# Performance work log

Measured on AMD Instinct MI355X. Metric: run time of the kernel, lower is better.

The kernel has to match this reference:

```python
import jax, jax.numpy as jnp
import numpy as np

N, E, F_IN, H, D = 50000, 800000, 256, 4, 128


def _gat_layer(x, W, al, ar, bias, src, dst):
    # x: [N, Fin]; W: [Fin, H*D]; al/ar: [H, D]; bias: [H*D]
    feat = (x @ W).reshape(N, H, D)                      # [N,H,D]
    el = jnp.einsum('nhd,hd->nh', feat, al)              # [N,H]
    er = jnp.einsum('nhd,hd->nh', feat, ar)              # [N,H]
    e = jax.nn.leaky_relu(el[src] + er[dst], negative_slope=0.2)  # [E,H]
    # edge softmax over incoming edges of each dst node (numerically stable)
    emax = jax.ops.segment_max(e, dst, num_segments=N)   # [N,H]
    ee = jnp.exp(e - emax[dst])                          # [E,H]
    denom = jax.ops.segment_sum(ee, dst, num_segments=N) # [N,H]
    a = ee / denom[dst]                                  # [E,H]
    # weighted scatter-aggregate of source features
    out = jax.ops.segment_sum(feat[src] * a[:, :, None], dst, num_segments=N)  # [N,H,D]
    return out + bias.reshape(H, D)


def setup_inputs() -> dict:
    key = jax.random.key(0)
    ks = jax.random.split(key, 16)
    f32 = jnp.float32
    nfeats = jax.random.normal(ks[0], (N, F_IN), dtype=f32)
    src = jax.random.randint(ks[1], (E,), 0, N, dtype=jnp.int32)
    dst = jax.random.randint(ks[2], (E,), 0, N, dtype=jnp.int32)
    def lin(k, fin):
        return jax.random.normal(k, (fin, H * D), dtype=f32) / np.sqrt(fin).astype(np.float32)
    def attn(k):
        return jax.random.normal(k, (H, D), dtype=f32) / np.sqrt(D).astype(np.float32)
    return {
        'nfeats': nfeats,
        'W1': lin(ks[3], F_IN), 'al1': attn(ks[4]), 'ar1': attn(ks[5]), 'b1': jnp.zeros((H * D,), f32),
        'W2': lin(ks[6], D),    'al2': attn(ks[7]), 'ar2': attn(ks[8]), 'b2': jnp.zeros((H * D,), f32),
        'W3': lin(ks[9], D),    'al3': attn(ks[10]), 'ar3': attn(ks[11]), 'b3': jnp.zeros((H * D,), f32),
        'Wc': jax.random.normal(ks[12], (D, 1), dtype=f32) / np.sqrt(D).astype(np.float32),
        'bc': jnp.zeros((1,), f32),
        'src': src, 'dst': dst,
    }


def reference(nfeats, W1, al1, ar1, b1, W2, al2, ar2, b2, W3, al3, ar3, b3, Wc, bc, src, dst):
    h = jnp.mean(jax.nn.relu(_gat_layer(nfeats, W1, al1, ar1, b1, src, dst)), axis=1)  # [N,D]
    h = jnp.mean(jax.nn.relu(_gat_layer(h, W2, al2, ar2, b2, src, dst)), axis=1)
    h = jnp.mean(jax.nn.relu(_gat_layer(h, W3, al3, ar3, b3, src, dst)), axis=1)
    hg = jnp.mean(h, axis=0, keepdims=True)  # readout: mean over nodes -> [1,D]
    return jax.nn.sigmoid(hg @ Wc + bc)      # [1,1]
```

## Files before the change

kernel.cpp:

```cpp
#include <hip/hip_runtime.h>
#include <hip/hip_bf16.h>

#define N_NODES 50000
#define E_EDGES 800000
#define HD 512
#define H_HEADS 4
#define D_DIM 128
#define N_PAD 53248

typedef __attribute__((ext_vector_type(8))) short bf16x8;
typedef __attribute__((ext_vector_type(4))) float f32x4;
typedef __attribute__((ext_vector_type(2))) float f32x2;

__device__ __forceinline__ unsigned short f2b(float f) {
  unsigned u = __float_as_uint(f);
  u += 0x7FFFu + ((u >> 16) & 1u);
  return (unsigned short)(u >> 16);
}
__device__ __forceinline__ float b2f(unsigned short s) {
  return __uint_as_float(((unsigned)s) << 16);
}
__device__ __forceinline__ float lrelu(float v) { return v > 0.f ? v : 0.2f * v; }
__device__ __forceinline__ float sel4(float a, float b, float c, float d, int h) {
  return h == 0 ? a : (h == 1 ? b : (h == 2 ? c : d));
}
__device__ __forceinline__ float sel4v(float4 v, int h) {
  return sel4(v.x, v.y, v.z, v.w, h);
}

#define GLOAD_LDS16(g, l)                                             \
  __builtin_amdgcn_global_load_lds(                                   \
      (const __attribute__((address_space(1))) void*)(g),             \
      (__attribute__((address_space(3))) void*)(l), 16, 0, 0)

__global__ void cast_f2b(const float* __restrict__ in, unsigned short* __restrict__ out, int n4) {
  int i = blockIdx.x * blockDim.x + threadIdx.x;
  if (i >= n4) return;
  float4 v = *(const float4*)(in + (size_t)i * 4);
  ushort4 o;
  o.x = f2b(v.x); o.y = f2b(v.y); o.z = f2b(v.z); o.w = f2b(v.w);
  *(ushort4*)(out + (size_t)i * 4) = o;
}

__global__ void transpose_cast(const float* __restrict__ W, unsigned short* __restrict__ WT, int K) {
  int idx = blockIdx.x * blockDim.x + threadIdx.x;
  if (idx >= K * HD) return;
  int k = idx >> 9, c = idx & (HD - 1);
  WT[(size_t)c * K + k] = f2b(W[idx]);
}

__global__ __launch_bounds__(256) void gemm_mfma(const unsigned short* __restrict__ X,
                                                 const unsigned short* __restrict__ WT,
                                                 unsigned char* __restrict__ featq,
                                                 const float* __restrict__ al,
                                                 const float* __restrict__ ar,
                                                 float* __restrict__ el, float* __restrict__ er,
                                                 int K) {
  __shared__ unsigned short Atile[128 * 64];
  __shared__ unsigned short Btile[128 * 64];
  __shared__ float eds[2][2][128];
  const int tid = threadIdx.x;
  const int w = tid >> 6, l = tid & 63;
  const int wr = w >> 1, wc = w & 1;
  const int row0 = blockIdx.x * 128;
  const int h = blockIdx.y;
  const int col0 = h * 128;
  const int fr = l & 15;
  const int g = l >> 4;
  const int fk = g * 8;
  f32x4 acc[4][4] = {};

  for (int k0 = 0; k0 < K; k0 += 64) {
#pragma unroll
    for (int j = 0; j < 4; ++j) {
      int idx = j * 256 + tid;
      int row = idx >> 3;
      int ksw = ((idx & 7) << 3) ^ ((row & 7) << 3);
      int arow = row0 + row;
      if (arow >= N_NODES) arow = N_NODES - 1;
      GLOAD_LDS16(X + (size_t)arow * K + k0 + ksw,
                  (char*)Atile + j * 4096 + w * 1024);
      GLOAD_LDS16(WT + (size_t)(col0 + row) * K + k0 + ksw,
                  (char*)Btile + j * 4096 + w * 1024);
    }
    __syncthreads();
#pragma unroll
    for (int kk = 0; kk < 64; kk += 32) {
      const int kel2 = (kk + fk) * 2;
      bf16x8 af[4], bf[4];
#pragma unroll
      for (int m = 0; m < 4; ++m) {
        int arow = wr * 64 + m * 16 + fr;
        af[m] = *(const bf16x8*)((const char*)Atile + arow * 128 + (kel2 ^ ((arow & 7) << 4)));
        int bcol = wc * 64 + m * 16 + fr;
        bf[m] = *(const bf16x8*)((const char*)Btile + bcol * 128 + (kel2 ^ ((bcol & 7) << 4)));
      }
#pragma unroll
      for (int m = 0; m < 4; ++m)
#pragma unroll
        for (int n = 0; n < 4; ++n)
          acc[m][n] = __builtin_amdgcn_mfma_f32_16x16x32_bf16(af[m], bf[n], acc[m][n], 0, 0, 0);
    }
    __syncthreads();
  }

  const int col_base = col0 + wc * 64;
#pragma unroll
  for (int m = 0; m < 4; ++m) {
#pragma unroll
    for (int i = 0; i < 4; ++i) {
      int r = row0 + wr * 64 + m * 16 + g * 4 + i;
      if (r < N_NODES) {
#pragma unroll
        for (int n = 0; n < 4; ++n) {
          int b = __builtin_amdgcn_cvt_pk_fp8_f32(acc[m][n][i], acc[m][n][i], 0, false);
          featq[(size_t)r * HD + col_base + n * 16 + fr] = (unsigned char)(b & 0xFF);
        }
      }
    }
  }

  float alk[4], ark[4];
#pragma unroll
  for (int n = 0; n < 4; ++n) {
    int c = wc * 64 + n * 16 + fr;
    alk[n] = al[h * D_DIM + c];
    ark[n] = ar[h * D_DIM + c];
  }
#pragma unroll
  for (int m = 0; m < 4; ++m) {
#pragma unroll
    for (int i = 0; i < 4; ++i) {
      float pel = 0.f, per = 0.f;
#pragma unroll
      for (int n = 0; n < 4; ++n) {
        pel = fmaf(acc[m][n][i], alk[n], pel);
        per = fmaf(acc[m][n][i], ark[n], per);
      }
#pragma unroll
      for (int o = 1; o < 16; o <<= 1) {
        pel += __shfl_xor(pel, o);
        per += __shfl_xor(per, o);
      }
      if (fr == 0) {
        int rloc = wr * 64 + m * 16 + g * 4 + i;
        eds[0][wc][rloc] = pel;
        eds[1][wc][rloc] = per;
      }
    }
  }
  __syncthreads();
  if (tid < 128) {
    int r = row0 + tid;
    if (r < N_NODES) {
      el[(size_t)r * 4 + h] = eds[0][0][tid] + eds[0][1][tid];
      er[(size_t)r * 4 + h] = eds[1][0][tid] + eds[1][1][tid];
    }
  }
}

__global__ void histo_kernel(const int* __restrict__ dst, unsigned* __restrict__ deg) {
  int e = blockIdx.x * blockDim.x + threadIdx.x;
  if (e >= E_EDGES) return;
  atomicAdd(&deg[dst[e]], 1u);
}

__global__ void scan_kernel(const unsigned* __restrict__ deg, unsigned* __restrict__ off,
                            unsigned* __restrict__ cursor) {
  __shared__ unsigned warp_sums[16];
  __shared__ unsigned carry_s;
  const int tid = threadIdx.x;
  const int wid = tid >> 6;
  if (tid == 0) carry_s = 0;
  __syncthreads();
  for (int base = 0; base < N_PAD; base += 4096) {
    int i = base + tid * 4;
    uint4 v = *(const uint4*)(deg + i);
    unsigned sm = v.x + v.y + v.z + v.w;
    unsigned x = sm;
#pragma unroll
    for (int o = 1; o < 64; o <<= 1) {
      unsigned y = __shfl_up(x, o);
      if ((tid & 63) >= o) x += y;
    }
    if ((tid & 63) == 63) warp_sums[wid] = x;
    __syncthreads();
    if (tid < 16) {
      unsigned s = warp_sums[tid];
#pragma unroll
      for (int o = 1; o < 16; o <<= 1) {
        unsigned y = __shfl_up(s, o);
        if (tid >= o) s += y;
      }
      warp_sums[tid] = s;
    }
    __syncthreads();
    unsigned carry = carry_s;
    unsigned wprev = (wid > 0) ? warp_sums[wid - 1] : 0u;
    unsigned ex = carry + wprev + (x - sm);
    uint4 o4;
    o4.x = ex;
    o4.y = ex + v.x;
    o4.z = o4.y + v.y;
    o4.w = o4.z + v.z;
    *(uint4*)(off + i) = o4;
    *(uint4*)(cursor + i) = o4;
    __syncthreads();
    if (tid == 0) carry_s = carry + warp_sums[15];
    __syncthreads();
  }
}

__global__ void scatter_kernel(const int* __restrict__ src, const int* __restrict__ dst,
                               unsigned* __restrict__ cursor, int* __restrict__ csr_src) {
  int e = blockIdx.x * blockDim.x + threadIdx.x;
  if (e >= E_EDGES) return;
  int d = dst[e];
  unsigned pos = atomicAdd(&cursor[d], 1u);
  csr_src[pos] = src[e];
}

__global__ __launch_bounds__(64) void agg_fused(const unsigned* __restrict__ off,
                                                const int* __restrict__ csr_src,
                                                const float* __restrict__ el,
                                                const float* __restrict__ er,
                                                const unsigned char* __restrict__ featq,
                                                const float* __restrict__ bias,
                                                unsigned short* __restrict__ hbuf) {
  __shared__ float4 ws4[64];
  const int n = blockIdx.x, t = threadIdx.x;
  const int h = t >> 4, d0 = (t & 15) * 8;
  const unsigned beg = off[n];
  const int deg = (int)(off[n + 1] - beg);
  const float NEG = -3.0e38f;
  float4 rr = *(const float4*)(er + (size_t)n * 4);
  f32x2 acc2[4] = {};

  if (deg <= 64) {
    float4 v = {NEG, NEG, NEG, NEG};
    if (t < deg) {
      int s = csr_src[beg + t];
      float4 ll = *(const float4*)(el + (size_t)s * 4);
      v.x = lrelu(ll.x + rr.x);
      v.y = lrelu(ll.y + rr.y);
      v.z = lrelu(ll.z + rr.z);
      v.w = lrelu(ll.w + rr.w);
    }
    float m0 = v.x, m1 = v.y, m2 = v.z, m3 = v.w;
#pragma unroll
    for (int o = 32; o >= 1; o >>= 1) {
      m0 = fmaxf(m0, __shfl_xor(m0, o));
      m1 = fmaxf(m1, __shfl_xor(m1, o));
      m2 = fmaxf(m2, __shfl_xor(m2, o));
      m3 = fmaxf(m3, __shfl_xor(m3, o));
    }
    float4 ev = {0.f, 0.f, 0.f, 0.f};
    if (t < deg) {
      ev.x = __expf(v.x - m0);
      ev.y = __expf(v.y - m1);
      ev.z = __expf(v.z - m2);
      ev.w = __expf(v.w - m3);
    }
    float s0 = ev.x, s1 = ev.y, s2 = ev.z, s3 = ev.w;
#pragma unroll
    for (int o = 32; o >= 1; o >>= 1) {
      s0 += __shfl_xor(s0, o);
      s1 += __shfl_xor(s1, o);
      s2 += __shfl_xor(s2, o);
      s3 += __shfl_xor(s3, o);
    }
    ws4[t] = ev;
    float invh = 1.0f / sel4(s0, s1, s2, s3, h);
    __syncthreads();
    const unsigned char* fq = featq + t * 8;
    for (int j0 = 0; j0 < deg; j0 += 4) {
      int i1 = (j0 + 1 < deg) ? j0 + 1 : j0;
      int i2 = (j0 + 2 < deg) ? j0 + 2 : j0;
      int i3 = (j0 + 3 < deg) ? j0 + 3 : j0;
      int sa = csr_src[beg + j0], sb = csr_src[beg + i1];
      int sc = csr_src[beg + i2], sd = csr_src[beg + i3];
      uint2 qa = *(const uint2*)(fq + (size_t)sa * HD);
      uint2 qb = *(const uint2*)(fq + (size_t)sb * HD);
      uint2 qc = *(const uint2*)(fq + (size_t)sc * HD);
      uint2 qd = *(const uint2*)(fq + (size_t)sd * HD);
      float wa = sel4v(ws4[j0], h) * invh;
      float wb = sel4v(ws4[i1], h) * invh;
      float wc2 = sel4v(ws4[i2], h) * invh;
      float wd = sel4v(ws4[i3], h) * invh;
      if (j0 + 1 >= deg) wb = 0.f;
      if (j0 + 2 >= deg) wc2 = 0.f;
      if (j0 + 3 >= deg) wd = 0.f;
      f32x2 w2;
      w2 = (f32x2){wa, wa};
      acc2[0] += __builtin_amdgcn_cvt_pk_f32_fp8((int)qa.x, false) * w2;
      acc2[1] += __builtin_amdgcn_cvt_pk_f32_fp8((int)qa.x, true) * w2;
      acc2[2] += __builtin_amdgcn_cvt_pk_f32_fp8((int)qa.y, false) * w2;
      acc2[3] += __builtin_amdgcn_cvt_pk_f32_fp8((int)qa.y, true) * w2;
      w2 = (f32x2){wb, wb};
      acc2[0] += __builtin_amdgcn_cvt_pk_f32_fp8((int)qb.x, false) * w2;
      acc2[1] += __builtin_amdgcn_cvt_pk_f32_fp8((int)qb.x, true) * w2;
      acc2[2] += __builtin_amdgcn_cvt_pk_f32_fp8((int)qb.y, false) * w2;
      acc2[3] += __builtin_amdgcn_cvt_pk_f32_fp8((int)qb.y, true) * w2;
      w2 = (f32x2){wc2, wc2};
      acc2[0] += __builtin_amdgcn_cvt_pk_f32_fp8((int)qc.x, false) * w2;
      acc2[1] += __builtin_amdgcn_cvt_pk_f32_fp8((int)qc.x, true) * w2;
      acc2[2] += __builtin_amdgcn_cvt_pk_f32_fp8((int)qc.y, false) * w2;
      acc2[3] += __builtin_amdgcn_cvt_pk_f32_fp8((int)qc.y, true) * w2;
      w2 = (f32x2){wd, wd};
      acc2[0] += __builtin_amdgcn_cvt_pk_f32_fp8((int)qd.x, false) * w2;
      acc2[1] += __builtin_amdgcn_cvt_pk_f32_fp8((int)qd.x, true) * w2;
      acc2[2] += __builtin_amdgcn_cvt_pk_f32_fp8((int)qd.y, false) * w2;
      acc2[3] += __builtin_amdgcn_cvt_pk_f32_fp8((int)qd.y, true) * w2;
    }
  } else {
    float m[4] = {NEG, NEG, NEG, NEG};
    for (int j = t; j < deg; j += 64) {
      int s = csr_src[beg + j];
      float4 ll = *(const float4*)(el + (size_t)s * 4);
      m[0] = fmaxf(m[0], lrelu(ll.x + rr.x));
      m[1] = fmaxf(m[1], lrelu(ll.y + rr.y));
      m[2] = fmaxf(m[2], lrelu(ll.z + rr.z));
      m[3] = fmaxf(m[3], lrelu(ll.w + rr.w));
    }
#pragma unroll
    for (int o = 32; o >= 1; o >>= 1) {
      m[0] = fmaxf(m[0], __shfl_xor(m[0], o));
      m[1] = fmaxf(m[1], __shfl_xor(m[1], o));
      m[2] = fmaxf(m[2], __shfl_xor(m[2], o));
      m[3] = fmaxf(m[3], __shfl_xor(m[3], o));
    }
    float sm[4] = {0.f, 0.f, 0.f, 0.f};
    for (int j = t; j < deg; j += 64) {
      int s = csr_src[beg + j];
      float4 ll = *(const float4*)(el + (size_t)s * 4);
      sm[0] += __expf(lrelu(ll.x + rr.x) - m[0]);
      sm[1] += __expf(lrelu(ll.y + rr.y) - m[1]);
      sm[2] += __expf(lrelu(ll.z + rr.z) - m[2]);
      sm[3] += __expf(lrelu(ll.w + rr.w) - m[3]);
    }
#pragma unroll
    for (int o = 32; o >= 1; o >>= 1) {
      sm[0] += __shfl_xor(sm[0], o);
      sm[1] += __shfl_xor(sm[1], o);
      sm[2] += __shfl_xor(sm[2], o);
      sm[3] += __shfl_xor(sm[3], o);
    }
    float mh = sel4(m[0], m[1], m[2], m[3], h);
    float ih = 1.0f / sel4(sm[0], sm[1], sm[2], sm[3], h);
    float rrh = sel4(rr.x, rr.y, rr.z, rr.w, h);
    for (int j = 0; j < deg; ++j) {
      int sj = csr_src[beg + j];
      float llh = el[(size_t)sj * 4 + h];
      float w = __expf(lrelu(llh + rrh) - mh) * ih;
      uint2 q = *(const uint2*)(featq + (size_t)sj * HD + t * 8);
      f32x2 w2 = {w, w};
      acc2[0] += __builtin_amdgcn_cvt_pk_f32_fp8((int)q.x, false) * w2;
      acc2[1] += __builtin_amdgcn_cvt_pk_f32_fp8((int)q.x, true) * w2;
      acc2[2] += __builtin_amdgcn_cvt_pk_f32_fp8((int)q.y, false) * w2;
      acc2[3] += __builtin_amdgcn_cvt_pk_f32_fp8((int)q.y, true) * w2;
    }
  }

  const float* bp = bias + h * D_DIM + d0;
  float4 b0 = *(const float4*)bp, b1 = *(const float4*)(bp + 4);
  float bv[8] = {b0.x, b0.y, b0.z, b0.w, b1.x, b1.y, b1.z, b1.w};
  float r[8];
#pragma unroll
  for (int i = 0; i < 8; ++i) r[i] = fmaxf(acc2[i >> 1][i & 1] + bv[i], 0.f);
#pragma unroll
  for (int i = 0; i < 8; ++i) {
    r[i] += __shfl_xor(r[i], 16);
    r[i] += __shfl_xor(r[i], 32);
  }
  if (h == 0) {
    uint4 o;
    o.x = (unsigned)f2b(r[0] * 0.25f) | ((unsigned)f2b(r[1] * 0.25f) << 16);
    o.y = (unsigned)f2b(r[2] * 0.25f) | ((unsigned)f2b(r[3] * 0.25f) << 16);
    o.z = (unsigned)f2b(r[4] * 0.25f) | ((unsigned)f2b(r[5] * 0.25f) << 16);
    o.w = (unsigned)f2b(r[6] * 0.25f) | ((unsigned)f2b(r[7] * 0.25f) << 16);
    *(uint4*)(hbuf + (size_t)n * D_DIM + d0) = o;
  }
}

__global__ void colsum(const unsigned short* __restrict__ hbuf, float* __restrict__ hg) {
  int d = threadIdx.x;
  float s = 0.0f;
  for (int n = blockIdx.x; n < N_NODES; n += gridDim.x)
    s += b2f(hbuf[(size_t)n * D_DIM + d]);
  atomicAdd(&hg[d], s);
}

__global__ void final_k(const float* __restrict__ hg, const float* __restrict__ Wc,
                        const float* __restrict__ bc, float* __restrict__ out) {
  int l = threadIdx.x;
  float v = hg[l] * Wc[l] + hg[l + 64] * Wc[l + 64];
#pragma unroll
  for (int off = 32; off >= 1; off >>= 1) v += __shfl_xor(v, off);
  if (l == 0) {
    float x = v * (1.0f / N_NODES) + bc[0];
    out[0] = 1.0f / (1.0f + expf(-x));
  }
}

extern "C" void kernel_launch(void* const* d_in, const int* in_sizes, int n_in,
                              void* d_out, int out_size, void* d_ws, size_t ws_size,
                              hipStream_t stream) {
  const float* nfeats = (const float*)d_in[0];
  const float* W1 = (const float*)d_in[1];
  const float* al1 = (const float*)d_in[2];
  const float* ar1 = (const float*)d_in[3];
  const float* b1 = (const float*)d_in[4];
  const float* W2 = (const float*)d_in[5];
  const float* al2 = (const float*)d_in[6];
  const float* ar2 = (const float*)d_in[7];
  const float* b2 = (const float*)d_in[8];
  const float* W3 = (const float*)d_in[9];
  const float* al3 = (const float*)d_in[10];
  const float* ar3 = (const float*)d_in[11];
  const float* b3 = (const float*)d_in[12];
  const float* Wc = (const float*)d_in[13];
  const float* bc = (const float*)d_in[14];
  const int* src = (const int*)d_in[15];
  const int* dst = (const int*)d_in[16];
  float* out = (float*)d_out;

  char* p = (char*)d_ws;
  auto carve = [&](size_t bytes) {
    char* r = p;
    p += (bytes + 255) & ~(size_t)255;
    return r;
  };
  float* el = (float*)carve((size_t)N_NODES * 4 * 4);
  float* er = (float*)carve((size_t)N_NODES * 4 * 4);
  float* hg = (float*)carve(512);
  unsigned* deg = (unsigned*)carve((size_t)N_PAD * 4);
  unsigned* offv = (unsigned*)carve((size_t)(N_PAD + 4) * 4);
  unsigned* cursor = (unsigned*)carve((size_t)N_PAD * 4);
  int* csr_src = (int*)carve((size_t)E_EDGES * 4);
  unsigned char* featq = (unsigned char*)carve((size_t)N_NODES * HD);
  unsigned short* hbufb = (unsigned short*)carve((size_t)N_NODES * D_DIM * 2);
  unsigned short* xb = (unsigned short*)carve((size_t)(N_NODES + 128) * 256 * 2);
  unsigned short* WT1 = (unsigned short*)carve((size_t)HD * 256 * 2);
  unsigned short* WT2 = (unsigned short*)carve((size_t)HD * 128 * 2);
  unsigned short* WT3 = (unsigned short*)carve((size_t)HD * 128 * 2);

  hipMemsetAsync(deg, 0, (size_t)N_PAD * sizeof(unsigned), stream);
  histo_kernel<<<(E_EDGES + 255) / 256, 256, 0, stream>>>(dst, deg);
  scan_kernel<<<1, 1024, 0, stream>>>(deg, offv, cursor);
  scatter_kernel<<<(E_EDGES + 255) / 256, 256, 0, stream>>>(src, dst, cursor, csr_src);

  cast_f2b<<<(N_NODES * 256 / 4 + 255) / 256, 256, 0, stream>>>(nfeats, xb, N_NODES * 256 / 4);
  transpose_cast<<<(256 * HD + 255) / 256, 256, 0, stream>>>(W1, WT1, 256);
  transpose_cast<<<(128 * HD + 255) / 256, 256, 0, stream>>>(W2, WT2, 128);
  transpose_cast<<<(128 * HD + 255) / 256, 256, 0, stream>>>(W3, WT3, 128);

  auto run_layer = [&](const unsigned short* X, int K, const unsigned short* WT,
                       const float* alv, const float* arv, const float* bv) {
    dim3 g((N_NODES + 127) / 128, H_HEADS);
    gemm_mfma<<<g, 256, 0, stream>>>(X, WT, featq, alv, arv, el, er, K);
    agg_fused<<<N_NODES, 64, 0, stream>>>(offv, csr_src, el, er, featq, bv, hbufb);
  };

  run_layer(xb, 256, WT1, al1, ar1, b1);
  run_layer(hbufb, 128, WT2, al2, ar2, b2);
  run_layer(hbufb, 128, WT3, al3, ar3, b3);

  hipMemsetAsync(hg, 0, 512, stream);
  colsum<<<1024, 128, 0, stream>>>(hbufb, hg);
  final_k<<<1, 64, 0, stream>>>(hg, Wc, bc, out);
}
```

Baseline: 466.2 us.

## Widen GEMM tiles to two heads per block, parallelize scan, merge weight casts

The GEMM now uses 512-thread blocks that each compute a 128x256 output tile covering two heads, so each A tile is loaded once per two heads instead of once per head. The el/er reduction is rewritten to handle both heads. The single-block serial scan is split into a multi-block local scan, a scan of block sums and an add pass. The three weight transpose/cast launches are merged into one. The larger tile raises LDS use and register pressure per block, and the scan now needs two extra launches.

```diff
diff --git a/kernel.cpp b/kernel.cpp
--- a/kernel.cpp
+++ b/kernel.cpp
@@ -42,14 +42,29 @@
   *(ushort4*)(out + (size_t)i * 4) = o;
 }
 
-__global__ void transpose_cast(const float* __restrict__ W, unsigned short* __restrict__ WT, int K) {
+__global__ void transpose_cast_all(const float* __restrict__ W1, const float* __restrict__ W2,
+                                   const float* __restrict__ W3,
+                                   unsigned short* __restrict__ WT1,
+                                   unsigned short* __restrict__ WT2,
+                                   unsigned short* __restrict__ WT3) {
   int idx = blockIdx.x * blockDim.x + threadIdx.x;
-  if (idx >= K * HD) return;
-  int k = idx >> 9, c = idx & (HD - 1);
-  WT[(size_t)c * K + k] = f2b(W[idx]);
-}
-
-__global__ __launch_bounds__(256) void gemm_mfma(const unsigned short* __restrict__ X,
+  const float* W;
+  unsigned short* WT;
+  int K, base;
+  if (idx < 131072) {
+    W = W1; WT = WT1; K = 256; base = idx;
+  } else if (idx < 196608) {
+    W = W2; WT = WT2; K = 128; base = idx - 131072;
+  } else if (idx < 262144) {
+    W = W3; WT = WT3; K = 128; base = idx - 196608;
+  } else {
+    return;
+  }
+  int k = base / HD, c = base & (HD - 1);
+  WT[(size_t)c * K + k] = f2b(W[(size_t)k * HD + c]);
+}
+
+__global__ __launch_bounds__(512) void gemm_mfma(const unsigned short* __restrict__ X,
                                                  const unsigned short* __restrict__ WT,
                                                  unsigned char* __restrict__ featq,
                                                  const float* __restrict__ al,
@@ -57,14 +72,14 @@
                                                  float* __restrict__ el, float* __restrict__ er,
                                                  int K) {
   __shared__ unsigned short Atile[128 * 64];
-  __shared__ unsigned short Btile[128 * 64];
-  __shared__ float eds[2][2][128];
+  __shared__ unsigned short Btile[256 * 64];
+  __shared__ float eds[2][2][2][128];
   const int tid = threadIdx.x;
   const int w = tid >> 6, l = tid & 63;
-  const int wr = w >> 1, wc = w & 1;
+  const int wr = w >> 2, wc = w & 3;
   const int row0 = blockIdx.x * 128;
-  const int h = blockIdx.y;
-  const int col0 = h * 128;
+  const int by = blockIdx.y;
+  const int col0 = by * 256;
   const int fr = l & 15;
   const int g = l >> 4;
   const int fk = g * 8;
@@ -72,16 +87,22 @@
 
   for (int k0 = 0; k0 < K; k0 += 64) {
 #pragma unroll
-    for (int j = 0; j < 4; ++j) {
-      int idx = j * 256 + tid;
+    for (int j = 0; j < 2; ++j) {
+      int idx = j * 512 + tid;
       int row = idx >> 3;
       int ksw = ((idx & 7) << 3) ^ ((row & 7) << 3);
       int arow = row0 + row;
       if (arow >= N_NODES) arow = N_NODES - 1;
       GLOAD_LDS16(X + (size_t)arow * K + k0 + ksw,
-                  (char*)Atile + j * 4096 + w * 1024);
+                  (char*)Atile + j * 8192 + w * 1024);
+    }
+#pragma unroll
+    for (int j = 0; j < 4; ++j) {
+      int idx = j * 512 + tid;
+      int row = idx >> 3;
+      int ksw = ((idx & 7) << 3) ^ ((row & 7) << 3);
       GLOAD_LDS16(WT + (size_t)(col0 + row) * K + k0 + ksw,
-                  (char*)Btile + j * 4096 + w * 1024);
+                  (char*)Btile + j * 8192 + w * 1024);
     }
     __syncthreads();
 #pragma unroll
@@ -104,7 +125,6 @@
     __syncthreads();
   }
 
-  const int col_base = col0 + wc * 64;
 #pragma unroll
   for (int m = 0; m < 4; ++m) {
 #pragma unroll
@@ -114,18 +134,20 @@
 #pragma unroll
         for (int n = 0; n < 4; ++n) {
           int b = __builtin_amdgcn_cvt_pk_fp8_f32(acc[m][n][i], acc[m][n][i], 0, false);
-          featq[(size_t)r * HD + col_base + n * 16 + fr] = (unsigned char)(b & 0xFF);
+          featq[(size_t)r * HD + col0 + wc * 64 + n * 16 + fr] = (unsigned char)(b & 0xFF);
         }
       }
     }
   }
 
+  const int hl = wc >> 1, half = wc & 1;
+  const int h = by * 2 + hl;
   float alk[4], ark[4];
 #pragma unroll
   for (int n = 0; n < 4; ++n) {
-    int c = wc * 64 + n * 16 + fr;
-    alk[n] = al[h * D_DIM + c];
-    ark[n] = ar[h * D_DIM + c];
+    int c = h * D_DIM + half * 64 + n * 16 + fr;
+    alk[n] = al[c];
+    ark[n] = ar[c];
   }
 #pragma unroll
   for (int m = 0; m < 4; ++m) {
@@ -144,17 +166,20 @@
       }
       if (fr == 0) {
         int rloc = wr * 64 + m * 16 + g * 4 + i;
-        eds[0][wc][rloc] = pel;
-        eds[1][wc][rloc] = per;
+        eds[0][half][hl][rloc] = pel;
+        eds[1][half][hl][rloc] = per;
       }
     }
   }
   __syncthreads();
-  if (tid < 128) {
-    int r = row0 + tid;
+  {
+    int row = tid >> 2, q = tid & 3;
+    int hl2 = q & 1, sel = q >> 1;
+    int r = row0 + row;
     if (r < N_NODES) {
-      el[(size_t)r * 4 + h] = eds[0][0][tid] + eds[0][1][tid];
-      er[(size_t)r * 4 + h] = eds[1][0][tid] + eds[1][1][tid];
+      float v = eds[sel][0][hl2][row] + eds[sel][1][hl2][row];
+      float* dst = (sel ? er : el);
+      dst[(size_t)r * 4 + by * 2 + hl2] = v;
     }
   }
 }
@@ -165,50 +190,63 @@
   atomicAdd(&deg[dst[e]], 1u);
 }
 
-__global__ void scan_kernel(const unsigned* __restrict__ deg, unsigned* __restrict__ off,
-                            unsigned* __restrict__ cursor) {
+__global__ void scan_local(const unsigned* __restrict__ deg, unsigned* __restrict__ off,
+                           unsigned* __restrict__ bsum) {
   __shared__ unsigned warp_sums[16];
-  __shared__ unsigned carry_s;
   const int tid = threadIdx.x;
   const int wid = tid >> 6;
-  if (tid == 0) carry_s = 0;
+  int i = blockIdx.x * 4096 + tid * 4;
+  uint4 v = *(const uint4*)(deg + i);
+  unsigned sm = v.x + v.y + v.z + v.w;
+  unsigned x = sm;
+#pragma unroll
+  for (int o = 1; o < 64; o <<= 1) {
+    unsigned y = __shfl_up(x, o);
+    if ((tid & 63) >= o) x += y;
+  }
+  if ((tid & 63) == 63) warp_sums[wid] = x;
   __syncthreads();
-  for (int base = 0; base < N_PAD; base += 4096) {
-    int i = base + tid * 4;
-    uint4 v = *(const uint4*)(deg + i);
-    unsigned sm = v.x + v.y + v.z + v.w;
-    unsigned x = sm;
-#pragma unroll
-    for (int o = 1; o < 64; o <<= 1) {
-      unsigned y = __shfl_up(x, o);
-      if ((tid & 63) >= o) x += y;
-    }
-    if ((tid & 63) == 63) warp_sums[wid] = x;
-    __syncthreads();
-    if (tid < 16) {
-      unsigned s = warp_sums[tid];
-#pragma unroll
-      for (int o = 1; o < 16; o <<= 1) {
-        unsigned y = __shfl_up(s, o);
-        if (tid >= o) s += y;
-      }
-      warp_sums[tid] = s;
-    }
-    __syncthreads();
-    unsigned carry = carry_s;
-    unsigned wprev = (wid > 0) ? warp_sums[wid - 1] : 0u;
-    unsigned ex = carry + wprev + (x - sm);
-    uint4 o4;
-    o4.x = ex;
-    o4.y = ex + v.x;
-    o4.z = o4.y + v.y;
-    o4.w = o4.z + v.z;
-    *(uint4*)(off + i) = o4;
-    *(uint4*)(cursor + i) = o4;
-    __syncthreads();
-    if (tid == 0) carry_s = carry + warp_sums[15];
-    __syncthreads();
-  }
+  if (tid < 16) {
+    unsigned s = warp_sums[tid];
+#pragma unroll
+    for (int o = 1; o < 16; o <<= 1) {
+      unsigned y = __shfl_up(s, o);
+      if (tid >= o) s += y;
+    }
+    warp_sums[tid] = s;
+  }
+  __syncthreads();
+  unsigned wprev = (wid > 0) ? warp_sums[wid - 1] : 0u;
+  unsigned ex = wprev + (x - sm);
+  uint4 o4;
+  o4.x = ex;
+  o4.y = ex + v.x;
+  o4.z = o4.y + v.y;
+  o4.w = o4.z + v.z;
+  *(uint4*)(off + i) = o4;
+  if (tid == 1023) bsum[blockIdx.x] = warp_sums[15];
+}
+
+__global__ void scan_bsums(unsigned* __restrict__ bsum) {
+  int t = threadIdx.x;
+  unsigned v = (t < 13) ? bsum[t] : 0u;
+  unsigned x = v;
+#pragma unroll
+  for (int o = 1; o < 16; o <<= 1) {
+    unsigned y = __shfl_up(x, o);
+    if (t >= o) x += y;
+  }
+  if (t < 13) bsum[t] = x - v;
+}
+
+__global__ void scan_add(unsigned* __restrict__ off, const unsigned* __restrict__ bsum,
+                         unsigned* __restrict__ cursor) {
+  int i = (blockIdx.x * 1024 + threadIdx.x) * 4;
+  unsigned p = bsum[blockIdx.x >> 2];
+  uint4 v = *(const uint4*)(off + i);
+  v.x += p; v.y += p; v.z += p; v.w += p;
+  *(uint4*)(off + i) = v;
+  *(uint4*)(cursor + i) = v;
 }
 
 __global__ void scatter_kernel(const int* __restrict__ src, const int* __restrict__ dst,
@@ -436,6 +474,7 @@
   unsigned* deg = (unsigned*)carve((size_t)N_PAD * 4);
   unsigned* offv = (unsigned*)carve((size_t)(N_PAD + 4) * 4);
   unsigned* cursor = (unsigned*)carve((size_t)N_PAD * 4);
+  unsigned* bsum = (unsigned*)carve(64 * 4);
   int* csr_src = (int*)carve((size_t)E_EDGES * 4);
   unsigned char* featq = (unsigned char*)carve((size_t)N_NODES * HD);
   unsigned short* hbufb = (unsigned short*)carve((size_t)N_NODES * D_DIM * 2);
@@ -446,18 +485,18 @@
 
   hipMemsetAsync(deg, 0, (size_t)N_PAD * sizeof(unsigned), stream);
   histo_kernel<<<(E_EDGES + 255) / 256, 256, 0, stream>>>(dst, deg);
-  scan_kernel<<<1, 1024, 0, stream>>>(deg, offv, cursor);
+  scan_local<<<13, 1024, 0, stream>>>(deg, offv, bsum);
+  scan_bsums<<<1, 64, 0, stream>>>(bsum);
+  scan_add<<<13, 1024, 0, stream>>>(offv, bsum, cursor);
   scatter_kernel<<<(E_EDGES + 255) / 256, 256, 0, stream>>>(src, dst, cursor, csr_src);
 
   cast_f2b<<<(N_NODES * 256 / 4 + 255) / 256, 256, 0, stream>>>(nfeats, xb, N_NODES * 256 / 4);
-  transpose_cast<<<(256 * HD + 255) / 256, 256, 0, stream>>>(W1, WT1, 256);
-  transpose_cast<<<(128 * HD + 255) / 256, 256, 0, stream>>>(W2, WT2, 128);
-  transpose_cast<<<(128 * HD + 255) / 256, 256, 0, stream>>>(W3, WT3, 128);
+  transpose_cast_all<<<(262144 + 255) / 256, 256, 0, stream>>>(W1, W2, W3, WT1, WT2, WT3);
 
   auto run_layer = [&](const unsigned short* X, int K, const unsigned short* WT,
                        const float* alv, const float* arv, const float* bv) {
-    dim3 g((N_NODES + 127) / 128, H_HEADS);
-    gemm_mfma<<<g, 256, 0, stream>>>(X, WT, featq, alv, arv, el, er, K);
+    dim3 g((N_NODES + 127) / 128, 2);
+    gemm_mfma<<<g, 512, 0, stream>>>(X, WT, featq, alv, arv, el, er, K);
     agg_fused<<<N_NODES, 64, 0, stream>>>(offv, csr_src, el, er, featq, bv, hbufb);
   };
 
```

Result: slower. 790.8 us (+69.6%).
